# Kernel optimization log

Hardware: AMD Instinct MI355X
Metric: run time of the kernel (lower is better)

Reference implementation:

```python
import jax, jax.numpy as jnp
import numpy as np

D = 1024
H = 8
B, S = 4, 2048


def setup_inputs() -> dict:
    key = jax.random.key(0)
    ks = jax.random.split(key, 11)
    s = 0.02
    return {
        "Q": jax.random.normal(ks[0], (B, S, D), jnp.float32),
        "K": jax.random.normal(ks[1], (B, S, D), jnp.float32),
        "V": jax.random.normal(ks[2], (B, S, D), jnp.float32),
        "WQ": jax.random.normal(ks[3], (D, D), jnp.float32) * s,
        "bQ": jax.random.normal(ks[4], (D,), jnp.float32) * s,
        "WK": jax.random.normal(ks[5], (D, D), jnp.float32) * s,
        "bK": jax.random.normal(ks[6], (D,), jnp.float32) * s,
        "WV": jax.random.normal(ks[7], (D, D), jnp.float32) * s,
        "bV": jax.random.normal(ks[8], (D,), jnp.float32) * s,
        "Wl": jax.random.normal(ks[9], (D, D * H), jnp.float32) * s,
        "bl": jax.random.normal(ks[10], (D,), jnp.float32) * s,
    }


def reference(Q, K, V, WQ, bQ, WK, bK, WV, bV, Wl, bl):
    # SelfAttention (weights shared across all heads in the original module)
    q = Q @ WQ.T + bQ  # [B,S,D]
    k = K @ WK.T + bK
    v = V @ WV.T + bV
    scale = 1.0 / np.sqrt(D).astype(np.float32)
    scores = jnp.einsum('bqd,bkd->bqk', q, k) * scale  # [B,S,S]
    attn = jax.nn.softmax(scores, axis=-1)
    Z = jnp.einsum('bqk,bkd->bqd', attn, v)  # [B,S,D]
    # concat of H identical copies, then linear(D*H -> D)
    Zcat = jnp.tile(Z, (1, 1, H))  # [B,S,D*H]
    return Zcat @ Wl.T + bl
```

## Files before the change

### kernel.cpp

```cpp
#include <hip/hip_runtime.h>
#include <stdint.h>

#define DEV __device__ __forceinline__

typedef __attribute__((ext_vector_type(8))) unsigned short frag8;
typedef __attribute__((ext_vector_type(4))) float f32x4;
typedef __attribute__((ext_vector_type(8))) unsigned short ushort8;
typedef __attribute__((ext_vector_type(4))) unsigned short ushort4v;

DEV unsigned short f2bf(float f) {
  union { float f; unsigned u; } x; x.f = f;
  unsigned r = x.u + 0x7fffu + ((x.u >> 16) & 1u);
  return (unsigned short)(r >> 16);
}
DEV float bf2f(unsigned short b) {
  union { unsigned u; float f; } x; x.u = ((unsigned)b) << 16;
  return x.f;
}

DEV void gload_lds16(const void* g, void* l) {
  __builtin_amdgcn_global_load_lds((const __attribute__((address_space(1))) void*)g,
                                   (__attribute__((address_space(3))) void*)l, 16, 0, 0);
}

DEV void mfma_bf16(f32x4& c, frag8 a, frag8 b) {
  asm("v_mfma_f32_16x16x32_bf16 %0, %1, %2, %0" : "+v"(c) : "v"(a), "v"(b));
}

DEV void wait_vm8_barrier() {
  asm volatile("s_waitcnt vmcnt(8)" ::: "memory");
  __builtin_amdgcn_s_barrier();
  __builtin_amdgcn_sched_barrier(0);
}
DEV void wait_vm0_barrier() {
  asm volatile("s_waitcnt vmcnt(0)" ::: "memory");
  __builtin_amdgcn_s_barrier();
  __builtin_amdgcn_sched_barrier(0);
}
DEV void raw_barrier() {
  __builtin_amdgcn_s_barrier();
  __builtin_amdgcn_sched_barrier(0);
}

template<int BIAS, int MODE>
__global__ __launch_bounds__(256)
void gemm_bt(const unsigned short* __restrict__ A,
             const unsigned short* __restrict__ Bm,
             const float* __restrict__ bias0, const float* __restrict__ bias1,
             const float* __restrict__ bias2,
             float* __restrict__ rowsum,
             void* __restrict__ Cv,
             int N, int K, float scale,
             long sA, long sB, long sC,
             int nx, int ny)
{
  __shared__ unsigned short lds[2][2][128 * 64];

  const int tid  = threadIdx.x;
  const int lane = tid & 63;
  const int wave = tid >> 6;
  const int wm   = wave >> 1;
  const int wn   = wave & 1;

  const unsigned nwg = gridDim.x;
  const unsigned orig = blockIdx.x;
  const unsigned qq = nwg >> 3, rr = nwg & 7;
  const unsigned xcd = orig & 7, jj = orig >> 3;
  const unsigned wg = (xcd < rr ? xcd * (qq + 1) : rr * (qq + 1) + (xcd - rr) * qq) + jj;
  const unsigned bx = wg % (unsigned)nx;
  const unsigned tt = wg / (unsigned)nx;
  const unsigned by = tt % (unsigned)ny;
  const unsigned bz = tt / (unsigned)ny;

  const int bm = (int)by * 128;
  const int bn = (int)bx * 128;

  A  += (size_t)bz * (size_t)sA;
  Bm += (size_t)bz * (size_t)sB;

  const int r8  = lane >> 3;
  const int l8  = lane & 7;
  const int swz = ((l8 ^ r8) << 4);
  const size_t Kb = (size_t)K * 2;

  const char* gA = (const char*)A  + (size_t)(bm + wave * 32 + r8) * Kb + swz;
  const char* gB = (const char*)Bm + (size_t)(bn + wave * 32 + r8) * Kb + swz;
  char* lA0 = (char*)&lds[0][0][0] + wave * 32 * 128;
  char* lB0 = (char*)&lds[0][1][0] + wave * 32 * 128;
  char* lA1 = (char*)&lds[1][0][0] + wave * 32 * 128;
  char* lB1 = (char*)&lds[1][1][0] + wave * 32 * 128;

  const int cr = lane & 15;
  const int kq = lane >> 4;
  const int base16 = ((kq ^ (cr & 7)) << 4);
  const char* rA0 = (const char*)&lds[0][0][0] + (wm * 64 + cr) * 128;
  const char* rB0 = (const char*)&lds[0][1][0] + (wn * 64 + cr) * 128;
  const char* rA1 = (const char*)&lds[1][0][0] + (wm * 64 + cr) * 128;
  const char* rB1 = (const char*)&lds[1][1][0] + (wn * 64 + cr) * 128;

  f32x4 acc[4][4];
  #pragma unroll
  for (int m = 0; m < 4; ++m)
    #pragma unroll
    for (int n = 0; n < 4; ++n)
      acc[m][n] = f32x4{0.f, 0.f, 0.f, 0.f};

  auto STAGE = [&](int t, char* la, char* lb) {
    const char* ga = gA + (size_t)t * 128;
    const char* gb = gB + (size_t)t * 128;
    gload_lds16(ga,               la);
    gload_lds16(gb,               lb);
    gload_lds16(ga +  8 * Kb,     la + 1024);
    gload_lds16(gb +  8 * Kb,     lb + 1024);
    gload_lds16(ga + 16 * Kb,     la + 2048);
    gload_lds16(gb + 16 * Kb,     lb + 2048);
    gload_lds16(ga + 24 * Kb,     la + 3072);
    gload_lds16(gb + 24 * Kb,     lb + 3072);
  };
  auto COMPUTE = [&](const char* ra, const char* rb) {
    #pragma unroll
    for (int kk = 0; kk < 2; ++kk) {
      const int off = base16 ^ (kk << 6);
      frag8 a[4], b[4];
      #pragma unroll
      for (int f = 0; f < 4; ++f) {
        a[f] = *(const frag8*)(ra + f * 2048 + off);
        b[f] = *(const frag8*)(rb + f * 2048 + off);
      }
      #pragma unroll
      for (int m = 0; m < 4; ++m)
        #pragma unroll
        for (int n = 0; n < 4; ++n)
          mfma_bf16(acc[m][n], a[m], b[n]);
    }
  };

  const int nk = K >> 6;
  STAGE(0, lA0, lB0);
  for (int t = 0; t < nk; ++t) {
    const bool odd = t & 1;
    if (t + 1 < nk) {
      STAGE(t + 1, odd ? lA0 : lA1, odd ? lB0 : lB1);
      wait_vm8_barrier();
    } else {
      wait_vm0_barrier();
    }
    COMPUTE(odd ? rA1 : rA0, odd ? rB1 : rB0);
    raw_barrier();
  }

  const float* bias = bias0;
  if constexpr (MODE == 2) bias = (bz == 0) ? bias0 : (bz == 1) ? bias1 : bias2;

  #pragma unroll
  for (int m = 0; m < 4; ++m) {
    const int gr0 = bm + wm * 64 + m * 16 + kq * 4;
    float psum[4] = {0.f, 0.f, 0.f, 0.f};
    float inv0 = 1.f, inv1 = 1.f, inv2 = 1.f, inv3 = 1.f;
    if constexpr (MODE == 4) {
      const float4 rs = *(const float4*)&bias0[(size_t)bz * 2048 + gr0];
      inv0 = 1.f / rs.x; inv1 = 1.f / rs.y; inv2 = 1.f / rs.z; inv3 = 1.f / rs.w;
    }
    #pragma unroll
    for (int n = 0; n < 4; ++n) {
      const int gc = bn + wn * 64 + n * 16 + cr;
      float bb = 0.f;
      if constexpr (BIAS) bb = bias[gc];
      float v0 = acc[m][n][0], v1 = acc[m][n][1], v2 = acc[m][n][2], v3 = acc[m][n][3];
      v0 += bb; v1 += bb; v2 += bb; v3 += bb;
      if constexpr (MODE == 1) {
        float* C = (float*)Cv + (size_t)bz * (size_t)sC;
        C[(size_t)(gr0 + 0) * N + gc] = v0;
        C[(size_t)(gr0 + 1) * N + gc] = v1;
        C[(size_t)(gr0 + 2) * N + gc] = v2;
        C[(size_t)(gr0 + 3) * N + gc] = v3;
      } else if constexpr (MODE == 3) {
        unsigned short* C = (unsigned short*)Cv + (size_t)bz * (size_t)sC;
        unsigned short e0 = f2bf(__expf(v0 * scale));
        unsigned short e1 = f2bf(__expf(v1 * scale));
        unsigned short e2 = f2bf(__expf(v2 * scale));
        unsigned short e3 = f2bf(__expf(v3 * scale));
        C[(size_t)(gr0 + 0) * N + gc] = e0;
        C[(size_t)(gr0 + 1) * N + gc] = e1;
        C[(size_t)(gr0 + 2) * N + gc] = e2;
        C[(size_t)(gr0 + 3) * N + gc] = e3;
        psum[0] += bf2f(e0); psum[1] += bf2f(e1);
        psum[2] += bf2f(e2); psum[3] += bf2f(e3);
      } else if constexpr (MODE == 4) {
        unsigned short* C = (unsigned short*)Cv + (size_t)bz * (size_t)sC;
        C[(size_t)(gr0 + 0) * N + gc] = f2bf(v0 * inv0);
        C[(size_t)(gr0 + 1) * N + gc] = f2bf(v1 * inv1);
        C[(size_t)(gr0 + 2) * N + gc] = f2bf(v2 * inv2);
        C[(size_t)(gr0 + 3) * N + gc] = f2bf(v3 * inv3);
      } else if constexpr (MODE == 2) {
        if (bz == 2) {
          unsigned short* C = (unsigned short*)Cv + (size_t)2 * (size_t)sC;
          ushort4v u;
          u[0] = f2bf(v0); u[1] = f2bf(v1); u[2] = f2bf(v2); u[3] = f2bf(v3);
          *(ushort4v*)&C[((size_t)(gr0 >> 11) << 21) + (size_t)gc * 2048 + (gr0 & 2047)] = u;
        } else {
          unsigned short* C = (unsigned short*)Cv + (size_t)bz * (size_t)sC;
          C[(size_t)(gr0 + 0) * N + gc] = f2bf(v0);
          C[(size_t)(gr0 + 1) * N + gc] = f2bf(v1);
          C[(size_t)(gr0 + 2) * N + gc] = f2bf(v2);
          C[(size_t)(gr0 + 3) * N + gc] = f2bf(v3);
        }
      } else {
        unsigned short* C = (unsigned short*)Cv + (size_t)bz * (size_t)sC;
        C[(size_t)(gr0 + 0) * N + gc] = f2bf(v0);
        C[(size_t)(gr0 + 1) * N + gc] = f2bf(v1);
        C[(size_t)(gr0 + 2) * N + gc] = f2bf(v2);
        C[(size_t)(gr0 + 3) * N + gc] = f2bf(v3);
      }
    }
    if constexpr (MODE == 3) {
      #pragma unroll
      for (int j = 0; j < 4; ++j) {
        float p = psum[j];
        p += __shfl_xor(p, 1);
        p += __shfl_xor(p, 2);
        p += __shfl_xor(p, 4);
        p += __shfl_xor(p, 8);
        if (cr == 0) atomicAdd(&rowsum[(size_t)bz * 2048 + gr0 + j], p);
      }
    }
  }
}

__global__ __launch_bounds__(256)
void cvt3_bf16(const float* __restrict__ s0, const float* __restrict__ s1,
               const float* __restrict__ s2, unsigned short* __restrict__ out,
               int n8each)
{
  const float* src = (blockIdx.y == 0) ? s0 : (blockIdx.y == 1) ? s1 : s2;
  unsigned short* dst = out + (size_t)blockIdx.y * ((size_t)n8each * 8);
  int i = blockIdx.x * blockDim.x + threadIdx.x;
  const int stride = gridDim.x * blockDim.x;
  for (; i < n8each; i += stride) {
    const float4* p = (const float4*)src + (size_t)i * 2;
    float4 a = p[0], b = p[1];
    ushort8 o;
    o[0] = f2bf(a.x); o[1] = f2bf(a.y); o[2] = f2bf(a.z); o[3] = f2bf(a.w);
    o[4] = f2bf(b.x); o[5] = f2bf(b.y); o[6] = f2bf(b.z); o[7] = f2bf(b.w);
    *((ushort8*)dst + i) = o;
  }
}

__global__ __launch_bounds__(256)
void weff_kernel(const float* __restrict__ Wl, unsigned short* __restrict__ out)
{
  const int idx = blockIdx.x * 256 + threadIdx.x;
  const int j = idx >> 8;
  const int d = (idx & 255) << 2;
  float4 s = make_float4(0.f, 0.f, 0.f, 0.f);
  #pragma unroll
  for (int h = 0; h < 8; ++h) {
    float4 w = *(const float4*)&Wl[(size_t)j * 8192 + h * 1024 + d];
    s.x += w.x; s.y += w.y; s.z += w.z; s.w += w.w;
  }
  ushort4v o;
  o[0] = f2bf(s.x); o[1] = f2bf(s.y); o[2] = f2bf(s.z); o[3] = f2bf(s.w);
  *(ushort4v*)&out[(size_t)j * 1024 + d] = o;
}

__global__ __launch_bounds__(256)
void zero_f32(float* __restrict__ p, int n)
{
  const int i = blockIdx.x * 256 + threadIdx.x;
  if (i < n) p[i] = 0.f;
}

extern "C" void kernel_launch(void* const* d_in, const int* in_sizes, int n_in,
                              void* d_out, int out_size, void* d_ws, size_t ws_size,
                              hipStream_t stream)
{
  (void)in_sizes; (void)n_in; (void)out_size; (void)ws_size;

  const float* Q  = (const float*)d_in[0];
  const float* K  = (const float*)d_in[1];
  const float* V  = (const float*)d_in[2];
  const float* WQ = (const float*)d_in[3];
  const float* bQ = (const float*)d_in[4];
  const float* WK = (const float*)d_in[5];
  const float* bK = (const float*)d_in[6];
  const float* WV = (const float*)d_in[7];
  const float* bV = (const float*)d_in[8];
  const float* Wl = (const float*)d_in[9];
  const float* bl = (const float*)d_in[10];

  const size_t nX = (size_t)8192 * 1024;
  const size_t nW = (size_t)1024 * 1024;

  unsigned short* Qb  = (unsigned short*)d_ws;
  unsigned short* Vb  = Qb + 2 * nX;
  unsigned short* qb  = Vb + nX;
  unsigned short* vT  = qb + 2 * nX;
  unsigned short* Wqb = vT + nX;
  unsigned short* Wef = Wqb + 3 * nW;
  float*          rowsum = (float*)(Wef + nW);
  unsigned short* P   = Qb;
  unsigned short* kb  = qb + nX;
  unsigned short* Zb  = Vb;

  const int thr = 256;

  cvt3_bf16<<<dim3(1024, 3), thr, 0, stream>>>(Q, K, V, Qb, (int)(nX / 8));
  cvt3_bf16<<<dim3(512, 3),  thr, 0, stream>>>(WQ, WK, WV, Wqb, (int)(nW / 8));
  weff_kernel<<<1024, thr, 0, stream>>>(Wl, Wef);
  zero_f32<<<32, thr, 0, stream>>>(rowsum, 8192);

  gemm_bt<1, 2><<<1536, thr, 0, stream>>>(
      Qb, Wqb, bQ, bK, bV, nullptr, qb, 1024, 1024, 1.f,
      (long)nX, (long)nW, (long)nX, 8, 64);
  gemm_bt<0, 3><<<1024, thr, 0, stream>>>(
      qb, kb, nullptr, nullptr, nullptr, rowsum, P, 2048, 1024, 0.03125f,
      (long)(2048 * 1024), (long)(2048 * 1024), (long)(2048 * 2048), 16, 16);
  gemm_bt<0, 4><<<512, thr, 0, stream>>>(
      P, vT, rowsum, nullptr, nullptr, nullptr, Zb, 1024, 2048, 1.f,
      (long)(2048 * 2048), (long)(1024 * 2048), (long)(2048 * 1024), 8, 16);
  gemm_bt<1, 1><<<512, thr, 0, stream>>>(
      Zb, Wef, bl, nullptr, nullptr, nullptr, d_out, 1024, 1024, 1.f,
      0, 0, 0, 8, 64);
}
```

Before: 217.5 us.

## Fold Q/K weights and V/output weights algebraically to drop two large GEMMs

```diff
diff --git a/kernel.cpp b/kernel.cpp
--- a/kernel.cpp
+++ b/kernel.cpp
@@ -42,12 +42,11 @@
   __builtin_amdgcn_sched_barrier(0);
 }
 
-template<int BIAS, int MODE>
+template<int MODE>
 __global__ __launch_bounds__(256)
 void gemm_bt(const unsigned short* __restrict__ A,
              const unsigned short* __restrict__ Bm,
              const float* __restrict__ bias0, const float* __restrict__ bias1,
-             const float* __restrict__ bias2,
              float* __restrict__ rowsum,
              void* __restrict__ Cv,
              int N, int K, float scale,
@@ -149,9 +148,6 @@
     raw_barrier();
   }
 
-  const float* bias = bias0;
-  if constexpr (MODE == 2) bias = (bz == 0) ? bias0 : (bz == 1) ? bias1 : bias2;
-
   #pragma unroll
   for (int m = 0; m < 4; ++m) {
     const int gr0 = bm + wm * 64 + m * 16 + kq * 4;
@@ -164,22 +160,14 @@
     #pragma unroll
     for (int n = 0; n < 4; ++n) {
       const int gc = bn + wn * 64 + n * 16 + cr;
-      float bb = 0.f;
-      if constexpr (BIAS) bb = bias[gc];
       float v0 = acc[m][n][0], v1 = acc[m][n][1], v2 = acc[m][n][2], v3 = acc[m][n][3];
-      v0 += bb; v1 += bb; v2 += bb; v3 += bb;
-      if constexpr (MODE == 1) {
-        float* C = (float*)Cv + (size_t)bz * (size_t)sC;
-        C[(size_t)(gr0 + 0) * N + gc] = v0;
-        C[(size_t)(gr0 + 1) * N + gc] = v1;
-        C[(size_t)(gr0 + 2) * N + gc] = v2;
-        C[(size_t)(gr0 + 3) * N + gc] = v3;
-      } else if constexpr (MODE == 3) {
+      if constexpr (MODE == 3) {
+        const float c2v = bias0[(size_t)bz * (size_t)N + gc];
         unsigned short* C = (unsigned short*)Cv + (size_t)bz * (size_t)sC;
-        unsigned short e0 = f2bf(__expf(v0 * scale));
-        unsigned short e1 = f2bf(__expf(v1 * scale));
-        unsigned short e2 = f2bf(__expf(v2 * scale));
-        unsigned short e3 = f2bf(__expf(v3 * scale));
+        unsigned short e0 = f2bf(__expf((v0 + c2v) * scale));
+        unsigned short e1 = f2bf(__expf((v1 + c2v) * scale));
+        unsigned short e2 = f2bf(__expf((v2 + c2v) * scale));
+        unsigned short e3 = f2bf(__expf((v3 + c2v) * scale));
         C[(size_t)(gr0 + 0) * N + gc] = e0;
         C[(size_t)(gr0 + 1) * N + gc] = e1;
         C[(size_t)(gr0 + 2) * N + gc] = e2;
@@ -187,19 +175,20 @@
         psum[0] += bf2f(e0); psum[1] += bf2f(e1);
         psum[2] += bf2f(e2); psum[3] += bf2f(e3);
       } else if constexpr (MODE == 4) {
-        unsigned short* C = (unsigned short*)Cv + (size_t)bz * (size_t)sC;
-        C[(size_t)(gr0 + 0) * N + gc] = f2bf(v0 * inv0);
-        C[(size_t)(gr0 + 1) * N + gc] = f2bf(v1 * inv1);
-        C[(size_t)(gr0 + 2) * N + gc] = f2bf(v2 * inv2);
-        C[(size_t)(gr0 + 3) * N + gc] = f2bf(v3 * inv3);
-      } else if constexpr (MODE == 2) {
-        if (bz == 2) {
-          unsigned short* C = (unsigned short*)Cv + (size_t)2 * (size_t)sC;
+        const float bb = bias1[gc];
+        float* C = (float*)Cv + (size_t)bz * (size_t)sC;
+        C[(size_t)(gr0 + 0) * N + gc] = v0 * inv0 + bb;
+        C[(size_t)(gr0 + 1) * N + gc] = v1 * inv1 + bb;
+        C[(size_t)(gr0 + 2) * N + gc] = v2 * inv2 + bb;
+        C[(size_t)(gr0 + 3) * N + gc] = v3 * inv3 + bb;
+      } else if constexpr (MODE == 5) {
+        if (bz == 1) {
+          unsigned short* C = (unsigned short*)Cv + (size_t)sC;
           ushort4v u;
           u[0] = f2bf(v0); u[1] = f2bf(v1); u[2] = f2bf(v2); u[3] = f2bf(v3);
           *(ushort4v*)&C[((size_t)(gr0 >> 11) << 21) + (size_t)gc * 2048 + (gr0 & 2047)] = u;
         } else {
-          unsigned short* C = (unsigned short*)Cv + (size_t)bz * (size_t)sC;
+          unsigned short* C = (unsigned short*)Cv;
           C[(size_t)(gr0 + 0) * N + gc] = f2bf(v0);
           C[(size_t)(gr0 + 1) * N + gc] = f2bf(v1);
           C[(size_t)(gr0 + 2) * N + gc] = f2bf(v2);
@@ -247,6 +236,33 @@
 }
 
 __global__ __launch_bounds__(256)
+void tpose3(const float* __restrict__ s0, const float* __restrict__ s1,
+            const float* __restrict__ s2, unsigned short* __restrict__ wr)
+{
+  const int z = blockIdx.y;
+  const float* src = (z == 0) ? s0 : (z == 1) ? s1 : s2;
+  unsigned short* dst = wr + (size_t)((z == 0) ? 2 : (z == 1) ? 0 : 3) * 1024 * 1024;
+
+  __shared__ float t[64][65];
+  const int bx  = blockIdx.x & 15;
+  const int byy = blockIdx.x >> 4;
+  const int tx  = threadIdx.x & 63;
+  const int ty4 = threadIdx.x >> 6;
+
+  #pragma unroll
+  for (int i = 0; i < 16; ++i) {
+    const int r = i * 4 + ty4;
+    t[r][tx] = src[(size_t)(byy * 64 + r) * 1024 + bx * 64 + tx];
+  }
+  __syncthreads();
+  #pragma unroll
+  for (int i = 0; i < 16; ++i) {
+    const int r = i * 4 + ty4;
+    dst[(size_t)(bx * 64 + r) * 1024 + byy * 64 + tx] = f2bf(t[tx][r]);
+  }
+}
+
+__global__ __launch_bounds__(256)
 void weff_kernel(const float* __restrict__ Wl, unsigned short* __restrict__ out)
 {
   const int idx = blockIdx.x * 256 + threadIdx.x;
@@ -268,6 +284,60 @@
 {
   const int i = blockIdx.x * 256 + threadIdx.x;
   if (i < n) p[i] = 0.f;
+}
+
+__global__ __launch_bounds__(256)
+void u2_kernel(const float* __restrict__ WK, const float* __restrict__ bQ,
+               float* __restrict__ u2)
+{
+  const int k = blockIdx.x * 256 + threadIdx.x;
+  const int m0 = blockIdx.y * 256;
+  float a = 0.f;
+  for (int m = m0; m < m0 + 256; ++m)
+    a += WK[(size_t)m * 1024 + k] * bQ[m];
+  atomicAdd(&u2[k], a);
+}
+
+__global__ __launch_bounds__(256)
+void c2_kernel(const unsigned short* __restrict__ Kb, const float* __restrict__ u2,
+               float* __restrict__ c2)
+{
+  const int lane = threadIdx.x & 63;
+  const int w    = threadIdx.x >> 6;
+  const int r    = blockIdx.x * 4 + w;
+  const unsigned short* kr = Kb + (size_t)r * 1024 + lane * 16;
+  ushort8 a = *(const ushort8*)kr;
+  ushort8 b = *(const ushort8*)(kr + 8);
+  const float* uu = u2 + lane * 16;
+  float s = 0.f;
+  #pragma unroll
+  for (int i = 0; i < 8; ++i) s += bf2f(a[i]) * uu[i];
+  #pragma unroll
+  for (int i = 0; i < 8; ++i) s += bf2f(b[i]) * uu[8 + i];
+  #pragma unroll
+  for (int off = 32; off; off >>= 1) s += __shfl_xor(s, off);
+  if (lane == 0) c2[r] = s;
+}
+
+__global__ __launch_bounds__(256)
+void biasp_kernel(const unsigned short* __restrict__ Weffb, const float* __restrict__ bV,
+                  const float* __restrict__ bl, float* __restrict__ biasp)
+{
+  const int lane = threadIdx.x & 63;
+  const int w    = threadIdx.x >> 6;
+  const int j    = blockIdx.x * 4 + w;
+  const unsigned short* wr = Weffb + (size_t)j * 1024 + lane * 16;
+  ushort8 a = *(const ushort8*)wr;
+  ushort8 b = *(const ushort8*)(wr + 8);
+  const float* vv = bV + lane * 16;
+  float s = 0.f;
+  #pragma unroll
+  for (int i = 0; i < 8; ++i) s += bf2f(a[i]) * vv[i];
+  #pragma unroll
+  for (int i = 0; i < 8; ++i) s += bf2f(b[i]) * vv[8 + i];
+  #pragma unroll
+  for (int off = 32; off; off >>= 1) s += __shfl_xor(s, off);
+  if (lane == 0) biasp[j] = s + bl[j];
 }
 
 extern "C" void kernel_launch(void* const* d_in, const int* in_sizes, int n_in,
@@ -282,7 +352,7 @@
   const float* WQ = (const float*)d_in[3];
   const float* bQ = (const float*)d_in[4];
   const float* WK = (const float*)d_in[5];
-  const float* bK = (const float*)d_in[6];
+  const float* bK = (const float*)d_in[6];  (void)bK;
   const float* WV = (const float*)d_in[7];
   const float* bV = (const float*)d_in[8];
   const float* Wl = (const float*)d_in[9];
@@ -292,33 +362,41 @@
   const size_t nW = (size_t)1024 * 1024;
 
   unsigned short* Qb  = (unsigned short*)d_ws;
-  unsigned short* Vb  = Qb + 2 * nX;
-  unsigned short* qb  = Vb + nX;
-  unsigned short* vT  = qb + 2 * nX;
-  unsigned short* Wqb = vT + nX;
-  unsigned short* Wef = Wqb + 3 * nW;
-  float*          rowsum = (float*)(Wef + nW);
-  unsigned short* P   = Qb;
-  unsigned short* kb  = qb + nX;
-  unsigned short* Zb  = Vb;
+  unsigned short* Vb  = Qb + nX;
+  unsigned short* Kb  = Qb + 2 * nX;
+  unsigned short* qp  = Qb + 3 * nX;
+  unsigned short* vpT = Qb + 4 * nX;
+  unsigned short* Wr  = Qb + 5 * nX;
+  unsigned short* Weffb = Wr + nW;
+  unsigned short* WQt   = Wr + 2 * nW;
+  unsigned short* Tt    = Wr + 4 * nW;
+  float* Fv   = (float*)(Wr + 6 * nW);
+  float* rowsum = Fv;
+  float* u2     = Fv + 8192;
+  float* c2     = Fv + 9216;
+  float* biasp  = Fv + 17408;
+  unsigned short* P = Qb;
 
   const int thr = 256;
 
-  cvt3_bf16<<<dim3(1024, 3), thr, 0, stream>>>(Q, K, V, Qb, (int)(nX / 8));
-  cvt3_bf16<<<dim3(512, 3),  thr, 0, stream>>>(WQ, WK, WV, Wqb, (int)(nW / 8));
-  weff_kernel<<<1024, thr, 0, stream>>>(Wl, Wef);
-  zero_f32<<<32, thr, 0, stream>>>(rowsum, 8192);
-
-  gemm_bt<1, 2><<<1536, thr, 0, stream>>>(
-      Qb, Wqb, bQ, bK, bV, nullptr, qb, 1024, 1024, 1.f,
+  cvt3_bf16<<<dim3(1024, 3), thr, 0, stream>>>(Q, V, K, Qb, (int)(nX / 8));
+  tpose3<<<dim3(256, 3), thr, 0, stream>>>(WQ, WK, WV, Wr);
+  weff_kernel<<<1024, thr, 0, stream>>>(Wl, Weffb);
+  zero_f32<<<36, thr, 0, stream>>>(rowsum, 9216);
+  u2_kernel<<<dim3(4, 4), thr, 0, stream>>>(WK, bQ, u2);
+  biasp_kernel<<<256, thr, 0, stream>>>(Weffb, bV, bl, biasp);
+  c2_kernel<<<2048, thr, 0, stream>>>(Kb, u2, c2);
+
+  gemm_bt<0><<<128, thr, 0, stream>>>(
+      Wr, WQt, nullptr, nullptr, nullptr, Tt, 1024, 1024, 1.f,
+      (long)nW, (long)nW, (long)nW, 8, 8);
+  gemm_bt<5><<<1024, thr, 0, stream>>>(
+      Qb, Tt, nullptr, nullptr, nullptr, qp, 1024, 1024, 1.f,
       (long)nX, (long)nW, (long)nX, 8, 64);
-  gemm_bt<0, 3><<<1024, thr, 0, stream>>>(
-      qb, kb, nullptr, nullptr, nullptr, rowsum, P, 2048, 1024, 0.03125f,
+  gemm_bt<3><<<1024, thr, 0, stream>>>(
+      qp, Kb, c2, nullptr, rowsum, P, 2048, 1024, 0.03125f,
       (long)(2048 * 1024), (long)(2048 * 1024), (long)(2048 * 2048), 16, 16);
-  gemm_bt<0, 4><<<512, thr, 0, stream>>>(
-      P, vT, rowsum, nullptr, nullptr, nullptr, Zb, 1024, 2048, 1.f,
+  gemm_bt<4><<<512, thr, 0, stream>>>(
+      P, vpT, rowsum, biasp, nullptr, d_out, 1024, 2048, 1.f,
       (long)(2048 * 2048), (long)(1024 * 2048), (long)(2048 * 1024), 8, 16);
-  gemm_bt<1, 1><<<512, thr, 0, stream>>>(
-      Zb, Wef, bl, nullptr, nullptr, nullptr, d_out, 1024, 1024, 1.f,
-      0, 0, 0, 8, 64);
-}
+}
```

New measurement: 204.4 us. 1.06x faster.
